# Performance work log

Hardware: AMD Instinct MI355X
Metric: run time of the kernel (lower is better)

Reference implementation:

```python
import jax, jax.numpy as jnp
import numpy as np

H = 256  # hardcoded in the original module


def _contrast_map(img, w):
    """Faithful port of calculate_contrast_oneimg_l1.

    img: [B, C, 256, 256] -> [B, 256-2w, 256-2w, 120] (first 120 shift channels).
    """
    img = jnp.transpose(img, (0, 2, 3, 1))  # BHWC
    x_diff = img[:, w:H - w, w:H - w]       # center crop [B, H-2w, H-2w, C]
    # All (2w+1)^2 - 1 shifted abs-diff maps, summed over channels, in the
    # same (i, j) loop order as the torch double loop (center skipped).
    maps = [
        jnp.sum(jnp.abs(x_diff - img[:, w + i:H - w + i, w + j:H - w + j]), axis=3)
        for i in range(-w, w + 1)
        for j in range(-w, w + 1)
        if not (i == 0 and j == 0)
    ]
    x = jnp.stack(maps, axis=3)  # [B, H-2w, H-2w, (2w+1)^2 - 1]
    return jnp.abs(x[:, :, :, :120])


def setup_inputs() -> dict:
    key = jax.random.key(0)
    k1, k2 = jax.random.split(key)
    B, C = 16, 3
    return {
        "original_image": jax.random.uniform(k1, (B, C, H, H), dtype=jnp.float32),
        "simulated_image": jax.random.uniform(k2, (B, C, H, H), dtype=jnp.float32),
        "window_size": 5,
    }


def reference(original_image, simulated_image, window_size):
    c_orig = _contrast_map(original_image, window_size)
    c_sim = _contrast_map(simulated_image, window_size)
    # torch.nn.L1Loss() default reduction: mean abs diff
    return jnp.mean(jnp.abs(c_orig - c_sim))
```

## Files before the change

### kernel.cpp

```cpp
#include <hip/hip_runtime.h>

#define HH     256
#define PPITCH 280
#define PROWS  272
#define PPLANE (PPITCH * PROWS)
#define XOFF   12
#define YOFF   5

__device__ __forceinline__ unsigned sad8(unsigned a, unsigned b, unsigned c) {
  unsigned d;
  asm("v_sad_u8 %0, %1, %2, %3" : "=v"(d) : "v"(a), "v"(b), "v"(c));
  return d;
}
__device__ __forceinline__ unsigned sad32(unsigned a, unsigned b, unsigned c) {
  unsigned d;
  asm("v_sad_u32 %0, %1, %2, %3" : "=v"(d) : "v"(a), "v"(b), "v"(c));
  return d;
}
__device__ __forceinline__ unsigned mad24(unsigned a, unsigned b, unsigned c) {
  unsigned d;
  asm("v_mad_u32_u24 %0, %1, %2, %3" : "=v"(d) : "v"(a), "v"(b), "v"(c));
  return d;
}
__device__ __forceinline__ unsigned q8(float x) { return (unsigned)(x * 255.0f + 0.5f); }
__device__ __forceinline__ unsigned eld(uint4 v, int k) {
  return k == 0 ? v.x : k == 1 ? v.y : k == 2 ? v.z : v.w;
}
#define ELD(ARR, M) eld(ARR[(M) >> 2], (M) & 3)

__global__ __launch_bounds__(256, 4)
void pack_kernel(const float* __restrict__ orig, const float* __restrict__ sim,
                 unsigned* __restrict__ wimg) {
  const int id  = blockIdx.x * 256 + threadIdx.x;
  const int c4  = id & 63;
  const int row = (id >> 6) & 255;
  const int b   = (id >> 14) & 15;
  const int img = id >> 18;
  const float* base = (img ? sim : orig) + (size_t)b * 3 * HH * HH + row * HH + c4 * 4;
  float4 va = *(const float4*)(base);
  float4 vb = *(const float4*)(base + HH * HH);
  float4 vc = *(const float4*)(base + 2 * HH * HH);
  uint4 pk;
  pk.x = q8(va.x) | (q8(vb.x) << 8) | (q8(vc.x) << 16);
  pk.y = q8(va.y) | (q8(vb.y) << 8) | (q8(vc.y) << 16);
  pk.z = q8(va.z) | (q8(vb.z) << 8) | (q8(vc.z) << 16);
  pk.w = q8(va.w) | (q8(vb.w) << 8) | (q8(vc.w) << 16);
  wimg += (size_t)(img * 16 + b) * PPLANE + (row + YOFF) * PPITCH + XOFF + 4 * c4;
  *(uint4*)wimg = pk;
}

#define LOADR(S, RP)                                                        \
  { const uint4* q0_ = (const uint4*)(RP);                                  \
    const uint4* q1_ = (const uint4*)((RP) + 16 * PPLANE);                  \
    S##0[0]=q0_[0]; S##0[1]=q0_[1]; S##0[2]=q0_[2];                         \
    S##0[3]=q0_[3]; S##0[4]=q0_[4]; S##0[5]=q0_[5];                         \
    S##1[0]=q1_[0]; S##1[1]=q1_[1]; S##1[2]=q1_[2];                         \
    S##1[3]=q1_[3]; S##1[4]=q1_[4]; S##1[5]=q1_[5]; }

#define PF(S, P, J)                                                         \
  { unsigned so_ = sad8(cen0[P], ELD(S##0, (P)+(J)+8), zr);                 \
    unsigned ss_ = sad8(cen1[P], ELD(S##1, (P)+(J)+8), zr);                 \
    acc = sad32(so_, ss_, acc); }
#define PM(S, P, J)                                                         \
  { unsigned so_ = sad8(cen0[P], ELD(S##0, (P)+(J)+8), zr);                 \
    unsigned ss_ = sad8(cen1[P], ELD(S##1, (P)+(J)+8), zr);                 \
    unsigned d_  = sad32(so_, ss_, zr);                                     \
    unsigned w2_ = cenv[P] + (ym & xok[(P)+(J)+8]);                         \
    acc = mad24(d_, w2_, acc); }

#define JF(S,J) PF(S,0,J) PF(S,1,J) PF(S,2,J) PF(S,3,J)                     \
                PF(S,4,J) PF(S,5,J) PF(S,6,J) PF(S,7,J)
#define JM(S,J) PM(S,0,J) PM(S,1,J) PM(S,2,J) PM(S,3,J)                     \
                PM(S,4,J) PM(S,5,J) PM(S,6,J) PM(S,7,J)
#define ROWF(S) JF(S,-5) JF(S,-4) JF(S,-3) JF(S,-2) JF(S,-1) JF(S,0)        \
                JF(S,1) JF(S,2) JF(S,3) JF(S,4) JF(S,5)
#define ROWM(S) JM(S,-5) JM(S,-4) JM(S,-3) JM(S,-2) JM(S,-1) JM(S,0)        \
                JM(S,1) JM(S,2) JM(S,3) JM(S,4) JM(S,5)

__global__ __launch_bounds__(256, 2)
void contrast_main(const unsigned* __restrict__ wimg, float* __restrict__ out) {
  __shared__ float wsum[4];
  const int tid = threadIdx.x, lane = tid & 63, wv = tid >> 6;
  const int bx = blockIdx.x, by = blockIdx.y, b = blockIdx.z;
  const int lx = lane & 3, ly = lane >> 2;

  const int G   = by * 64 + wv * 16;
  const int y0  = G + ly - 5;
  const int xp0 = bx * 32 + 8 * lx - 5;

  const unsigned* rp = wimg + (size_t)b * PPLANE + (y0 + 5 + YOFF) * PPITCH
                     + bx * 32 + 8 * lx + 4;

  uint4 A0[6], A1[6], B0[6], B1[6];
  unsigned cen0[8], cen1[8];
  unsigned zr = 0, acc = 0;

  const bool fastw = (bx >= 1) && (bx <= 6) && (G >= 16) && (G <= 224);

  LOADR(A, rp)
  LOADR(B, rp + PPITCH)
  #pragma unroll
  for (int p = 0; p < 8; ++p) { cen0[p] = ELD(A0, p + 8); cen1[p] = ELD(A1, p + 8); }

  float ftot;
  if (fastw) {
    JF(A,1) JF(A,2) JF(A,3) JF(A,4) JF(A,5)
    const unsigned* pA = rp;
    const unsigned* pB = rp + PPITCH;
    #pragma unroll 1
    for (int t = 0; t < 2; ++t) {
      pA += 2 * PPITCH;
      LOADR(A, pA)
      ROWF(B)
      pB += 2 * PPITCH;
      LOADR(B, pB)
      ROWF(A)
    }
    ROWF(B)
    ftot = 2.0f * (float)acc;
  } else {
    unsigned xok[24];
    #pragma unroll
    for (int m = 0; m < 24; ++m)
      xok[m] = ((unsigned)(xp0 + m - 8) < 246u) ? 1u : 0u;
    const unsigned ym0v = ((unsigned)y0 < 246u) ? 1u : 0u;
    unsigned cenv[8];
    #pragma unroll
    for (int p = 0; p < 8; ++p) cenv[p] = ym0v & xok[p + 8];

    unsigned ym = ym0v;
    JM(A,1) JM(A,2) JM(A,3) JM(A,4) JM(A,5)
    const unsigned* pA = rp;
    const unsigned* pB = rp + PPITCH;
    #pragma unroll 1
    for (int t = 0; t < 2; ++t) {
      pA += 2 * PPITCH;
      LOADR(A, pA)
      ym = ((unsigned)(y0 + 2 * t + 1) < 246u) ? 1u : 0u;
      ROWM(B)
      pB += 2 * PPITCH;
      LOADR(B, pB)
      ym = ((unsigned)(y0 + 2 * t + 2) < 246u) ? 1u : 0u;
      ROWM(A)
    }
    ym = ((unsigned)(y0 + 5) < 246u) ? 1u : 0u;
    ROWM(B)
    ftot = (float)acc;
  }

  #pragma unroll
  for (int off = 32; off > 0; off >>= 1)
    ftot += __shfl_down(ftot, off, 64);
  if (lane == 0) wsum[wv] = ftot;
  __syncthreads();
  if (tid == 0) {
    const float scale = (1.0f / 255.0f) / 116190720.0f;
    atomicAdd(out, (wsum[0] + wsum[1] + wsum[2] + wsum[3]) * scale);
  }
}

extern "C" void kernel_launch(void* const* d_in, const int* in_sizes, int n_in,
                              void* d_out, int out_size, void* d_ws, size_t ws_size,
                              hipStream_t stream) {
  (void)in_sizes; (void)n_in; (void)ws_size; (void)out_size;
  const float* orig = (const float*)d_in[0];
  const float* sim  = (const float*)d_in[1];
  float* out = (float*)d_out;
  unsigned* wimg = (unsigned*)d_ws;

  hipMemsetAsync(out, 0, sizeof(float), stream);
  hipLaunchKernelGGL(pack_kernel, dim3(2048), dim3(256), 0, stream, orig, sim, wimg);
  hipLaunchKernelGGL(contrast_main, dim3(8, 4, 16), dim3(256), 0, stream, wimg, out);
}
```

Measured before the change: 91.24 us.

## Fuse uint8 packing into contrast kernel via per-block LDS tile

Removes the separate pack kernel and its global workspace round trip. Each block now loads its 69-row by 48-column halo tile of both images directly from the float inputs, quantizes and packs the three channels into LDS, and then reads its rows from LDS instead of global memory. Edge pixels are clamped rather than zero-padded, which is valid only because the masked path zeroes out-of-range contributions. This saves one launch and the workspace write and read, at the cost of redundant halo loads across blocks and extra LDS use per block.

```diff
diff --git a/kernel.cpp b/kernel.cpp
--- a/kernel.cpp
+++ b/kernel.cpp
@@ -1,11 +1,8 @@
 #include <hip/hip_runtime.h>
 
-#define HH     256
-#define PPITCH 280
-#define PROWS  272
-#define PPLANE (PPITCH * PROWS)
-#define XOFF   12
-#define YOFF   5
+#define HH 256
+#define LPITCH 52
+#define LROWS  69
 
 __device__ __forceinline__ unsigned sad8(unsigned a, unsigned b, unsigned c) {
   unsigned d;
@@ -28,30 +25,9 @@
 }
 #define ELD(ARR, M) eld(ARR[(M) >> 2], (M) & 3)
 
-__global__ __launch_bounds__(256, 4)
-void pack_kernel(const float* __restrict__ orig, const float* __restrict__ sim,
-                 unsigned* __restrict__ wimg) {
-  const int id  = blockIdx.x * 256 + threadIdx.x;
-  const int c4  = id & 63;
-  const int row = (id >> 6) & 255;
-  const int b   = (id >> 14) & 15;
-  const int img = id >> 18;
-  const float* base = (img ? sim : orig) + (size_t)b * 3 * HH * HH + row * HH + c4 * 4;
-  float4 va = *(const float4*)(base);
-  float4 vb = *(const float4*)(base + HH * HH);
-  float4 vc = *(const float4*)(base + 2 * HH * HH);
-  uint4 pk;
-  pk.x = q8(va.x) | (q8(vb.x) << 8) | (q8(vc.x) << 16);
-  pk.y = q8(va.y) | (q8(vb.y) << 8) | (q8(vc.y) << 16);
-  pk.z = q8(va.z) | (q8(vb.z) << 8) | (q8(vc.z) << 16);
-  pk.w = q8(va.w) | (q8(vb.w) << 8) | (q8(vc.w) << 16);
-  wimg += (size_t)(img * 16 + b) * PPLANE + (row + YOFF) * PPITCH + XOFF + 4 * c4;
-  *(uint4*)wimg = pk;
-}
-
-#define LOADR(S, RP)                                                        \
-  { const uint4* q0_ = (const uint4*)(RP);                                  \
-    const uint4* q1_ = (const uint4*)((RP) + 16 * PPLANE);                  \
+#define LOADR(S, R)                                                         \
+  { const uint4* q0_ = (const uint4*)&lds[0][R][8 * lx];                    \
+    const uint4* q1_ = (const uint4*)&lds[1][R][8 * lx];                    \
     S##0[0]=q0_[0]; S##0[1]=q0_[1]; S##0[2]=q0_[2];                         \
     S##0[3]=q0_[3]; S##0[4]=q0_[4]; S##0[5]=q0_[5];                         \
     S##1[0]=q1_[0]; S##1[1]=q1_[1]; S##1[2]=q1_[2];                         \
@@ -78,18 +54,47 @@
                 JM(S,1) JM(S,2) JM(S,3) JM(S,4) JM(S,5)
 
 __global__ __launch_bounds__(256, 2)
-void contrast_main(const unsigned* __restrict__ wimg, float* __restrict__ out) {
+void contrast_fused(const float* __restrict__ orig, const float* __restrict__ sim,
+                    float* __restrict__ out) {
+  __shared__ unsigned lds[2][LROWS][LPITCH];
   __shared__ float wsum[4];
   const int tid = threadIdx.x, lane = tid & 63, wv = tid >> 6;
   const int bx = blockIdx.x, by = blockIdx.y, b = blockIdx.z;
   const int lx = lane & 3, ly = lane >> 2;
 
-  const int G   = by * 64 + wv * 16;
+  const int G0 = by * 64;
+  const int c0base = bx * 32 - 8;
+  #pragma unroll
+  for (int i = 0; i < 7; ++i) {
+    int idx = i * 256 + tid;
+    if (idx < 2 * LROWS * 12) {
+      int q   = idx % 12;
+      int ri  = idx / 12;
+      int img = (ri >= LROWS) ? 1 : 0;
+      int r   = ri - img * LROWS;
+      int row = G0 + r;
+      if (row > 255) row = 255;
+      int col = c0base + 4 * q;
+      if (col < 0) col = 0;
+      if (col > 252) col = 252;
+      const float* p = (img ? sim : orig) + (size_t)b * 3 * HH * HH + row * HH + col;
+      float4 va = *(const float4*)(p);
+      float4 vb = *(const float4*)(p + HH * HH);
+      float4 vc = *(const float4*)(p + 2 * HH * HH);
+      uint4 pk;
+      pk.x = q8(va.x) | (q8(vb.x) << 8) | (q8(vc.x) << 16);
+      pk.y = q8(va.y) | (q8(vb.y) << 8) | (q8(vc.y) << 16);
+      pk.z = q8(va.z) | (q8(vb.z) << 8) | (q8(vc.z) << 16);
+      pk.w = q8(va.w) | (q8(vb.w) << 8) | (q8(vc.w) << 16);
+      *(uint4*)&lds[img][r][4 * q] = pk;
+    }
+  }
+  __syncthreads();
+
+  const int G   = G0 + wv * 16;
   const int y0  = G + ly - 5;
   const int xp0 = bx * 32 + 8 * lx - 5;
-
-  const unsigned* rp = wimg + (size_t)b * PPLANE + (y0 + 5 + YOFF) * PPITCH
-                     + bx * 32 + 8 * lx + 4;
+  const int rbase = wv * 16 + ly;
 
   uint4 A0[6], A1[6], B0[6], B1[6];
   unsigned cen0[8], cen1[8];
@@ -97,23 +102,19 @@
 
   const bool fastw = (bx >= 1) && (bx <= 6) && (G >= 16) && (G <= 224);
 
-  LOADR(A, rp)
-  LOADR(B, rp + PPITCH)
+  LOADR(A, rbase)
+  LOADR(B, rbase + 1)
   #pragma unroll
   for (int p = 0; p < 8; ++p) { cen0[p] = ELD(A0, p + 8); cen1[p] = ELD(A1, p + 8); }
 
   float ftot;
   if (fastw) {
     JF(A,1) JF(A,2) JF(A,3) JF(A,4) JF(A,5)
-    const unsigned* pA = rp;
-    const unsigned* pB = rp + PPITCH;
     #pragma unroll 1
     for (int t = 0; t < 2; ++t) {
-      pA += 2 * PPITCH;
-      LOADR(A, pA)
+      LOADR(A, rbase + 2 * t + 2)
       ROWF(B)
-      pB += 2 * PPITCH;
-      LOADR(B, pB)
+      LOADR(B, rbase + 2 * t + 3)
       ROWF(A)
     }
     ROWF(B)
@@ -130,16 +131,12 @@
 
     unsigned ym = ym0v;
     JM(A,1) JM(A,2) JM(A,3) JM(A,4) JM(A,5)
-    const unsigned* pA = rp;
-    const unsigned* pB = rp + PPITCH;
     #pragma unroll 1
     for (int t = 0; t < 2; ++t) {
-      pA += 2 * PPITCH;
-      LOADR(A, pA)
+      LOADR(A, rbase + 2 * t + 2)
       ym = ((unsigned)(y0 + 2 * t + 1) < 246u) ? 1u : 0u;
       ROWM(B)
-      pB += 2 * PPITCH;
-      LOADR(B, pB)
+      LOADR(B, rbase + 2 * t + 3)
       ym = ((unsigned)(y0 + 2 * t + 2) < 246u) ? 1u : 0u;
       ROWM(A)
     }
@@ -162,13 +159,11 @@
 extern "C" void kernel_launch(void* const* d_in, const int* in_sizes, int n_in,
                               void* d_out, int out_size, void* d_ws, size_t ws_size,
                               hipStream_t stream) {
-  (void)in_sizes; (void)n_in; (void)ws_size; (void)out_size;
+  (void)in_sizes; (void)n_in; (void)ws_size; (void)out_size; (void)d_ws;
   const float* orig = (const float*)d_in[0];
   const float* sim  = (const float*)d_in[1];
   float* out = (float*)d_out;
-  unsigned* wimg = (unsigned*)d_ws;
 
   hipMemsetAsync(out, 0, sizeof(float), stream);
-  hipLaunchKernelGGL(pack_kernel, dim3(2048), dim3(256), 0, stream, orig, sim, wimg);
-  hipLaunchKernelGGL(contrast_main, dim3(8, 4, 16), dim3(256), 0, stream, wimg, out);
+  hipLaunchKernelGGL(contrast_fused, dim3(8, 4, 16), dim3(256), 0, stream, orig, sim, out);
 }
```

After: 90.37 us. About the same (-0.9%).
